# Performance work log

Hardware: AMD Instinct MI355X
Metric: run time of the kernel (lower is better)

## Reference

```python
import jax, jax.numpy as jnp
import numpy as np
from jax import lax

B, L, T, CH, H = 32, 40960, 12, 512, 256  # batch, audio len, timestep, enc ch, gru hidden


def _conv_bn_relu(x, w, stride, pad, g, be):
    y = lax.conv_general_dilated(x, w, (stride,), [(pad, pad)],
                                 dimension_numbers=('NCH', 'OIH', 'NCH'))
    m = jnp.mean(y, axis=(0, 2), keepdims=True)          # train-mode BatchNorm1d
    v = jnp.var(y, axis=(0, 2), keepdims=True)
    y = (y - m) / jnp.sqrt(v + 1e-5) * g[None, :, None] + be[None, :, None]
    return jax.nn.relu(y)


def _gru(xs, wih, whh, bih, bhh):
    # xs: [B, F, I] -> outputs [B, F, H]; PyTorch GRU equations
    def step(h, x_t):
        gi = x_t @ wih.T + bih
        gh = h @ whh.T + bhh
        ir, iz, inn = jnp.split(gi, 3, axis=-1)
        hr, hz, hn = jnp.split(gh, 3, axis=-1)
        r = jax.nn.sigmoid(ir + hr)
        zg = jax.nn.sigmoid(iz + hz)
        n = jnp.tanh(inn + r * hn)
        h_new = (1 - zg) * n + zg * h
        return h_new, h_new
    h0 = jnp.zeros((xs.shape[0], whh.shape[1]), xs.dtype)
    _, ys = lax.scan(step, h0, jnp.swapaxes(xs, 0, 1))
    return jnp.swapaxes(ys, 0, 1)


def setup_inputs():
    ks = jax.random.split(jax.random.key(0), 16)
    x = jax.random.normal(ks[0], (B, 1, L), jnp.float32)
    seq_lens = jax.random.randint(ks[1], (B,), L // 2, L + 1)
    maxt = seq_lens // 160 - T                            # t ~ randint(seq_len/160 - timestep)
    u = jax.random.uniform(ks[2], (B,))
    t_samples = jnp.minimum((u * maxt).astype(jnp.int32), maxt - 1)
    d = {'x': x, 't_samples': t_samples}
    d['w1'] = jax.random.normal(ks[3], (CH, 1, 10), jnp.float32) * 0.1
    d['w2'] = jax.random.normal(ks[4], (CH, CH, 8), jnp.float32) * 0.03
    d['w3'] = jax.random.normal(ks[5], (CH, CH, 4), jnp.float32) * 0.05
    d['w4'] = jax.random.normal(ks[6], (CH, CH, 4), jnp.float32) * 0.05
    d['w5'] = jax.random.normal(ks[7], (CH, CH, 4), jnp.float32) * 0.05
    for i in range(5):
        d[f'g{i+1}'] = jnp.ones((CH,), jnp.float32)
        d[f'be{i+1}'] = jnp.zeros((CH,), jnp.float32)
    d['wih'] = jax.random.normal(ks[8], (3 * H, CH), jnp.float32) * 0.05
    d['whh'] = jax.random.normal(ks[9], (3 * H, H), jnp.float32) * 0.05
    d['bih'] = jnp.zeros((3 * H,), jnp.float32)
    d['bhh'] = jnp.zeros((3 * H,), jnp.float32)
    d['wk'] = jax.random.normal(ks[10], (T, CH, H), jnp.float32) * 0.05
    d['bk'] = jnp.zeros((T, CH), jnp.float32)
    return d


def reference(x, t_samples, w1, w2, w3, w4, w5, g1, g2, g3, g4, g5,
              be1, be2, be3, be4, be5, wih, whh, bih, bhh, wk, bk):
    z = _conv_bn_relu(x, w1, 5, 3, g1, be1)
    z = _conv_bn_relu(z, w2, 4, 2, g2, be2)
    z = _conv_bn_relu(z, w3, 2, 1, g3, be3)
    z = _conv_bn_relu(z, w4, 2, 1, g4, be4)
    z = _conv_bn_relu(z, w5, 2, 1, g5, be5)
    z = jnp.swapaxes(z, 1, 2)                              # [B, F, CH]
    # encode_samples: z at t+1 .. t+T  -> [T, B, CH]
    idx = t_samples[:, None] + jnp.arange(1, T + 1)[None, :]   # [B, T]
    enc = jnp.take_along_axis(z, idx[:, :, None], axis=1)      # [B, T, CH]
    enc = jnp.swapaxes(enc, 0, 1)                              # [T, B, CH]
    # zero-padded forward sequence (GRU is causal, so output at t only sees prefix)
    mask = (jnp.arange(z.shape[1])[None, :] <= t_samples[:, None]).astype(z.dtype)
    out = _gru(z * mask[:, :, None], wih, whh, bih, bhh)       # [B, F, H]
    c_t = out[jnp.arange(out.shape[0]), t_samples]             # [B, H]
    pred = jnp.einsum('bh,tdh->tbd', c_t, wk) + bk[:, None, :]  # [T, B, CH]
    totals = jnp.einsum('tbd,tcd->tbc', enc, pred)             # [T, B, B]
    lsm = jax.nn.log_softmax(totals, axis=2)                   # torch LogSoftmax dim=1 on 2D
    nce = jnp.trace(lsm, axis1=1, axis2=2).sum() / (-1.0 * B * T)
    preds = jnp.argmax(jax.nn.softmax(totals, axis=2), axis=1)  # argmax over dim 0 per column
    correct = jnp.sum(preds == jnp.arange(B)[None, :])
    accuracy = correct / B
    return (accuracy, nce)
```

## Files before the change

### kernel.cpp

```cpp
#include <hip/hip_runtime.h>
#include <hip/hip_bf16.h>


using bf16 = __hip_bfloat16;
typedef __attribute__((ext_vector_type(8))) short bf16x8;
typedef __attribute__((ext_vector_type(4))) float f32x4;

__device__ __forceinline__ float bf2f(bf16 v) { return __bfloat162float(v); }
__device__ __forceinline__ bf16 f2bf(float f) { return __float2bfloat16(f); }
__device__ __forceinline__ ushort bfbits(float f) {
  bf16 b = f2bf(f);
  return *reinterpret_cast<ushort*>(&b);
}
union FragU { uint4 u; bf16x8 v; };

__global__ __launch_bounds__(256) void stats1_kernel(
    const float* __restrict__ x, const float* __restrict__ w1, float* __restrict__ sums) {
  __shared__ float xs[2576];
  int s = blockIdx.x, b = blockIdx.y;
  const float* xb = x + (size_t)b * 40960;
  int w0 = 2560 * s - 3;
  for (int i = threadIdx.x; i < 2565; i += 256) {
    int xi = w0 + i;
    xs[i] = ((unsigned)xi < 40960u) ? xb[xi] : 0.f;
  }
  __syncthreads();
  int c0 = threadIdx.x, c1 = threadIdx.x + 256;
  float wA[10], wB[10];
#pragma unroll
  for (int k = 0; k < 10; ++k) { wA[k] = w1[c0 * 10 + k]; wB[k] = w1[c1 * 10 + k]; }
  float sA = 0.f, qA = 0.f, sB = 0.f, qB = 0.f;
  for (int f = 0; f < 512; ++f) {
    const float* xp = &xs[5 * f];
    float aA = 0.f, aB = 0.f;
#pragma unroll
    for (int k = 0; k < 10; ++k) {
      float xv = xp[k];
      aA = fmaf(xv, wA[k], aA);
      aB = fmaf(xv, wB[k], aB);
    }
    sA += aA; qA = fmaf(aA, aA, qA);
    sB += aB; qB = fmaf(aB, aB, qB);
  }
  atomicAdd(&sums[c0], sA); atomicAdd(&sums[512 + c0], qA);
  atomicAdd(&sums[c1], sB); atomicAdd(&sums[512 + c1], qB);
}

__global__ __launch_bounds__(256) void stats_kernel(
    const bf16* __restrict__ z, int F, float* __restrict__ sums) {
  int bc = blockIdx.x;
  int c = bc & 511;
  const bf16* p = z + (size_t)bc * F;
  float s = 0.f, q = 0.f;
  for (int i = threadIdx.x; i < F; i += 256) {
    float v = bf2f(p[i]);
    s += v;
    q = fmaf(v, v, q);
  }
  __shared__ float rs[256], rq[256];
  rs[threadIdx.x] = s; rq[threadIdx.x] = q;
  __syncthreads();
  for (int w = 128; w > 0; w >>= 1) {
    if (threadIdx.x < w) {
      rs[threadIdx.x] += rs[threadIdx.x + w];
      rq[threadIdx.x] += rq[threadIdx.x + w];
    }
    __syncthreads();
  }
  if (threadIdx.x == 0) {
    atomicAdd(&sums[c], rs[0]);
    atomicAdd(&sums[512 + c], rq[0]);
  }
}

__global__ void finalize_kernel(const float* __restrict__ sums, const float* __restrict__ g,
                                const float* __restrict__ be, float invN,
                                float* __restrict__ ab) {
  int c = threadIdx.x;
  float mean = sums[c] * invN;
  float var = fmaf(-mean, mean, sums[512 + c] * invN);
  float a = g[c] * rsqrtf(var + 1e-5f);
  ab[c] = a;
  ab[512 + c] = fmaf(-mean, a, be[c]);
}

__global__ __launch_bounds__(256) void transpose_kernel(
    const float* __restrict__ in, float* __restrict__ out, int R, int C) {
  __shared__ float t[64][65];
  int c0 = blockIdx.x * 64, r0 = blockIdx.y * 64;
  int tx = threadIdx.x & 63, ty = threadIdx.x >> 6;
  for (int i = ty; i < 64; i += 4) {
    int r = r0 + i, c = c0 + tx;
    t[i][tx] = (r < R && c < C) ? in[(size_t)r * C + c] : 0.f;
  }
  __syncthreads();
  for (int i = ty; i < 64; i += 4) {
    int c = c0 + i, r = r0 + tx;
    if (c < C && r < R) out[(size_t)c * R + r] = t[tx][i];
  }
}

__global__ void cvt_bf16_kernel(const float* __restrict__ in, bf16* __restrict__ out, int n) {
  int i = blockIdx.x * 256 + threadIdx.x;
  if (i < n) out[i] = f2bf(in[i]);
}

__global__ void pack_whh_kernel(const float* __restrict__ whh, uint* __restrict__ P) {
  int idx = blockIdx.x * 256 + threadIdx.x;
  if (idx < 98304) {
    int p = idx / 768, gj = idx % 768;
    float lo = whh[(size_t)gj * 256 + 2 * p];
    float hi = whh[(size_t)gj * 256 + 2 * p + 1];
    P[idx] = (uint)bfbits(lo) | ((uint)bfbits(hi) << 16);
  }
}

__global__ __launch_bounds__(256) void norm1_kernel(
    const float* __restrict__ x, const float* __restrict__ w1,
    const float* __restrict__ ab, bf16* __restrict__ zn, int chunk0) {
  __shared__ float xs[1312];
  int s = blockIdx.x, bl = blockIdx.y;
  int pidx = s * 256 + threadIdx.x;
  const float* xb = x + (size_t)(chunk0 + bl) * 40960;
  int w0 = 1280 * s - 33;
  for (int i = threadIdx.x; i < 1285; i += 256) {
    int xi = w0 + i;
    xs[i] = ((unsigned)xi < 40960u) ? xb[xi] : 0.f;
  }
  __syncthreads();
  if (pidx >= 8208) return;
  int fi = pidx - 6;
  bool inb = ((unsigned)fi < 8192u);
  const float* xp = &xs[5 * threadIdx.x];
  bf16* zp = zn + (size_t)bl * 512 * 8208 + pidx;
  for (int c = 0; c < 512; ++c) {
    float v = 0.f;
    if (inb) {
      float acc = 0.f;
      const float* w = &w1[c * 10];
#pragma unroll
      for (int k = 0; k < 10; ++k) acc = fmaf(xp[k], w[k], acc);
      v = fmaxf(fmaf(ab[c], acc, ab[512 + c]), 0.f);
    }
    zp[(size_t)c * 8208] = f2bf(v);
  }
}

__global__ __launch_bounds__(256) void conv2_mfma(
    const bf16* __restrict__ zn, const bf16* __restrict__ wB,
    bf16* __restrict__ out, int chunk0) {
  __shared__ ushort aL[4][520];
  __shared__ ushort bL[128][36];
  int fo0 = blockIdx.x * 128, co0 = blockIdx.y * 128, bl = blockIdx.z;
  int tid = threadIdx.x;
  int w = tid >> 6, l = tid & 63;
  int m0 = (w >> 1) * 64, n0 = (w & 1) * 64;
  int row = l & 15, kq = l >> 4;
  f32x4 acc[4][4];
#pragma unroll
  for (int i = 0; i < 4; ++i)
#pragma unroll
    for (int j = 0; j < 4; ++j) acc[i][j] = {0.f, 0.f, 0.f, 0.f};
  const ushort* zb = (const ushort*)zn + (size_t)bl * 512 * 8208;
  int astart = 4 * fo0 + 4;
  int sco = tid >> 1, shalf = tid & 1;
  for (int step = 0; step < 128; ++step) {
    int ci0 = step * 4;
    int k0 = step * 32;
    __syncthreads();
    for (int u = tid; u < 520; u += 256) {
      int ci = u / 130, off = (u % 130) * 4;
      *(uint2*)&aL[ci][off] =
          *(const uint2*)(zb + (size_t)(ci0 + ci) * 8208 + astart + off);
    }
    {
      const uint2* src = (const uint2*)(wB + (size_t)(co0 + sco) * 4096 + k0 + shalf * 16);
      uint2* dst = (uint2*)&bL[sco][shalf * 16];
      dst[0] = src[0]; dst[1] = src[1]; dst[2] = src[2]; dst[3] = src[3];
    }
    __syncthreads();
    bf16x8 af[4], bfr[4];
#pragma unroll
    for (int mi = 0; mi < 4; ++mi) {
      int am = (m0 + mi * 16 + row) * 4;
      const uint2* ap = (const uint2*)((const char*)&aL[0][0] + kq * 1040 + am * 2);
      uint2 a0 = ap[0], a1 = ap[1];
      FragU f; f.u = make_uint4(a0.x, a0.y, a1.x, a1.y);
      af[mi] = f.v;
    }
#pragma unroll
    for (int ni = 0; ni < 4; ++ni) {
      int col = n0 + ni * 16 + row;
      const uint2* bp = (const uint2*)((const char*)&bL[0][0] + col * 72 + kq * 16);
      uint2 b0 = bp[0], b1 = bp[1];
      FragU f; f.u = make_uint4(b0.x, b0.y, b1.x, b1.y);
      bfr[ni] = f.v;
    }
#pragma unroll
    for (int mi = 0; mi < 4; ++mi)
#pragma unroll
      for (int ni = 0; ni < 4; ++ni)
        acc[mi][ni] = __builtin_amdgcn_mfma_f32_16x16x32_bf16(af[mi], bfr[ni], acc[mi][ni], 0, 0, 0);
  }
  size_t ob = (size_t)(chunk0 + bl) * 512;
#pragma unroll
  for (int mi = 0; mi < 4; ++mi)
#pragma unroll
    for (int ni = 0; ni < 4; ++ni)
#pragma unroll
      for (int r = 0; r < 4; ++r) {
        int m = m0 + mi * 16 + kq * 4 + r;
        int n = n0 + ni * 16 + row;
        out[(ob + co0 + n) * 2048 + fo0 + m] = f2bf(acc[mi][ni][r]);
      }
}

__global__ __launch_bounds__(256) void convN_mfma(
    const bf16* __restrict__ in, const bf16* __restrict__ wB,
    const float* __restrict__ ab, bf16* __restrict__ out, int Fi, int Fo) {
  __shared__ ushort aL[8][264];
  __shared__ ushort bL[128][36];
  int fo0 = blockIdx.x * 128, co0 = blockIdx.y * 128, b = blockIdx.z;
  int tid = threadIdx.x;
  int w = tid >> 6, l = tid & 63;
  int m0 = (w >> 1) * 64, n0 = (w & 1) * 64;
  int row = l & 15, kq = l >> 4;
  f32x4 acc[4][4];
#pragma unroll
  for (int i = 0; i < 4; ++i)
#pragma unroll
    for (int j = 0; j < 4; ++j) acc[i][j] = {0.f, 0.f, 0.f, 0.f};
  int fi0 = fo0 * 2 - 1;
  const bf16* ib = in + (size_t)b * 512 * Fi;
  int sco = tid >> 1, shalf = tid & 1;
  for (int step = 0; step < 64; ++step) {
    int ci0 = step * 8;
    int k0 = step * 32;
    __syncthreads();
    for (int u = tid; u < 1032; u += 256) {
      int ci = u / 129, pp = (u % 129) * 2;
      float a = ab[ci0 + ci], bb = ab[512 + ci0 + ci];
      const bf16* zr = ib + (size_t)(ci0 + ci) * Fi;
      uint pk = 0;
#pragma unroll
      for (int e = 0; e < 2; ++e) {
        int fi = fi0 + pp + e;
        float v = 0.f;
        if ((unsigned)fi < (unsigned)Fi)
          v = fmaxf(fmaf(a, bf2f(zr[fi]), bb), 0.f);
        pk |= (uint)bfbits(v) << (16 * e);
      }
      *(uint*)&aL[ci][pp] = pk;
    }
    {
      const uint2* src = (const uint2*)(wB + (size_t)(co0 + sco) * 2048 + k0 + shalf * 16);
      uint2* dst = (uint2*)&bL[sco][shalf * 16];
      dst[0] = src[0]; dst[1] = src[1]; dst[2] = src[2]; dst[3] = src[3];
    }
    __syncthreads();
    bf16x8 af[4], bfr[4];
#pragma unroll
    for (int mi = 0; mi < 4; ++mi) {
      int p0 = (m0 + mi * 16 + row) * 2;
      const char* base = (const char*)&aL[0][0];
      const uint* r0p = (const uint*)(base + (2 * kq) * 528 + p0 * 2);
      const uint* r1p = (const uint*)(base + (2 * kq + 1) * 528 + p0 * 2);
      FragU f; f.u = make_uint4(r0p[0], r0p[1], r1p[0], r1p[1]);
      af[mi] = f.v;
    }
#pragma unroll
    for (int ni = 0; ni < 4; ++ni) {
      int col = n0 + ni * 16 + row;
      const uint2* bp = (const uint2*)((const char*)&bL[0][0] + col * 72 + kq * 16);
      uint2 b0 = bp[0], b1 = bp[1];
      FragU f; f.u = make_uint4(b0.x, b0.y, b1.x, b1.y);
      bfr[ni] = f.v;
    }
#pragma unroll
    for (int mi = 0; mi < 4; ++mi)
#pragma unroll
      for (int ni = 0; ni < 4; ++ni)
        acc[mi][ni] = __builtin_amdgcn_mfma_f32_16x16x32_bf16(af[mi], bfr[ni], acc[mi][ni], 0, 0, 0);
  }
  size_t ob = (size_t)b * 512;
#pragma unroll
  for (int mi = 0; mi < 4; ++mi)
#pragma unroll
    for (int ni = 0; ni < 4; ++ni)
#pragma unroll
      for (int r = 0; r < 4; ++r) {
        int m = m0 + mi * 16 + kq * 4 + r;
        int n = n0 + ni * 16 + row;
        out[(ob + co0 + n) * Fo + fo0 + m] = f2bf(acc[mi][ni][r]);
      }
}

__global__ __launch_bounds__(256) void gi_kernel(
    const bf16* __restrict__ z5, const float* __restrict__ wihT,
    const float* __restrict__ bih, const float* __restrict__ ab,
    float* __restrict__ gi) {
  __shared__ float a_lds[8][64];
  __shared__ float w_lds[8][128];
  int t0 = blockIdx.x * 64, j0 = blockIdx.y * 128, b = blockIdx.z;
  int tid = threadIdx.x, tx = tid & 15, ty = tid >> 4;
  float acc[4][8] = {};
  for (int ci0 = 0; ci0 < 512; ci0 += 8) {
    __syncthreads();
    for (int i = tid; i < 512; i += 256) {
      int ci = i >> 6, t = i & 63;
      float v = bf2f(z5[((size_t)b * 512 + ci0 + ci) * 256 + t0 + t]);
      a_lds[ci][t] = fmaxf(fmaf(ab[ci0 + ci], v, ab[512 + ci0 + ci]), 0.f);
    }
    {
      int i = tid * 4;
      int ci = i >> 7, j = i & 127;
      *(float4*)&w_lds[ci][j] = *(const float4*)&wihT[(size_t)(ci0 + ci) * 768 + j0 + j];
    }
    __syncthreads();
#pragma unroll
    for (int ci = 0; ci < 8; ++ci) {
      float av[4];
#pragma unroll
      for (int j = 0; j < 4; ++j) av[j] = a_lds[ci][tx + 16 * j];
      const float* wp = &w_lds[ci][ty * 8];
      float4 w0 = *(const float4*)wp;
      float4 w1 = *(const float4*)(wp + 4);
      float wv[8] = {w0.x, w0.y, w0.z, w0.w, w1.x, w1.y, w1.z, w1.w};
#pragma unroll
      for (int j = 0; j < 4; ++j)
#pragma unroll
        for (int cc = 0; cc < 8; ++cc)
          acc[j][cc] = fmaf(av[j], wv[cc], acc[j][cc]);
    }
  }
  float bv[8];
#pragma unroll
  for (int cc = 0; cc < 8; ++cc) bv[cc] = bih[j0 + ty * 8 + cc];
#pragma unroll
  for (int j = 0; j < 4; ++j) {
    int rowi = t0 + tx + 16 * j;
    float4 s0 = {acc[j][0] + bv[0], acc[j][1] + bv[1], acc[j][2] + bv[2], acc[j][3] + bv[3]};
    float4 s1 = {acc[j][4] + bv[4], acc[j][5] + bv[5], acc[j][6] + bv[6], acc[j][7] + bv[7]};
    float* gp = &gi[((size_t)b * 256 + rowi) * 768 + j0 + ty * 8];
    *(float4*)gp = s0;
    *(float4*)(gp + 4) = s1;
  }
}

__global__ __launch_bounds__(256) void gru_kernel(
    const float* __restrict__ gi, const uint* __restrict__ P,
    const float* __restrict__ bhh, const int* __restrict__ tsamp,
    float* __restrict__ c_t) {
  int b = blockIdx.x;
  int j = threadIdx.x;
  __shared__ float h[256];
  h[j] = 0.f;
  int Tb = tsamp[b];
  float bhr = bhh[j], bhz = bhh[256 + j], bhn = bhh[512 + j];
  const float* gib = gi + (size_t)b * 256 * 768;
  __syncthreads();
  for (int t = 0; t <= Tb; ++t) {
    const float* git = gib + t * 768;
    float dr = 0.f, dz = 0.f, dn = 0.f;
#pragma unroll 4
    for (int p = 0; p < 128; ++p) {
      uint ur = P[p * 768 + j];
      uint uz = P[p * 768 + 256 + j];
      uint un = P[p * 768 + 512 + j];
      float2 hh = *(const float2*)&h[2 * p];
      dr = fmaf(__uint_as_float(ur << 16), hh.x, dr);
      dr = fmaf(__uint_as_float(ur & 0xffff0000u), hh.y, dr);
      dz = fmaf(__uint_as_float(uz << 16), hh.x, dz);
      dz = fmaf(__uint_as_float(uz & 0xffff0000u), hh.y, dz);
      dn = fmaf(__uint_as_float(un << 16), hh.x, dn);
      dn = fmaf(__uint_as_float(un & 0xffff0000u), hh.y, dn);
    }
    float xr_ = git[j], xz_ = git[256 + j], xn_ = git[512 + j];
    float r = 1.f / (1.f + __expf(-(xr_ + dr + bhr)));
    float zg = 1.f / (1.f + __expf(-(xz_ + dz + bhz)));
    float n = tanhf(fmaf(r, dn + bhn, xn_));
    float hj = h[j];
    float hnew = fmaf(zg, hj - n, n);
    __syncthreads();
    h[j] = hnew;
    __syncthreads();
  }
  c_t[b * 256 + j] = h[j];
}

__global__ __launch_bounds__(256) void pred_kernel(
    const float* __restrict__ c_t, const float* __restrict__ wk,
    const float* __restrict__ bk, float* __restrict__ pred) {
  int tp = blockIdx.x >> 5, c = blockIdx.x & 31;
  __shared__ float cl[256];
  cl[threadIdx.x] = c_t[c * 256 + threadIdx.x];
  __syncthreads();
  const float* wkt = wk + (size_t)tp * 512 * 256;
  for (int d = threadIdx.x; d < 512; d += 256) {
    float a = bk[tp * 512 + d];
    const float* wv = wkt + (size_t)d * 256;
    for (int hh = 0; hh < 256; hh += 4) {
      float4 w4 = *(const float4*)&wv[hh];
      a = fmaf(w4.x, cl[hh], a);
      a = fmaf(w4.y, cl[hh + 1], a);
      a = fmaf(w4.z, cl[hh + 2], a);
      a = fmaf(w4.w, cl[hh + 3], a);
    }
    pred[((size_t)tp * 32 + c) * 512 + d] = a;
  }
}

__global__ __launch_bounds__(256) void totals_kernel(
    const bf16* __restrict__ z5, const float* __restrict__ ab,
    const int* __restrict__ tsamp, const float* __restrict__ pred,
    float* __restrict__ totals) {
  int tp = blockIdx.x >> 5, b = blockIdx.x & 31;
  __shared__ float el[512];
  __shared__ float red[256];
  int tb = tsamp[b] + 1 + tp;
  for (int d = threadIdx.x; d < 512; d += 256) {
    float v = bf2f(z5[((size_t)b * 512 + d) * 256 + tb]);
    el[d] = fmaxf(fmaf(ab[d], v, ab[512 + d]), 0.f);
  }
  __syncthreads();
  int c = threadIdx.x & 31, chunk = threadIdx.x >> 5;
  const float* pr = pred + ((size_t)tp * 32 + c) * 512 + chunk * 64;
  const float* ep = &el[chunk * 64];
  float a = 0.f;
#pragma unroll 8
  for (int d = 0; d < 64; ++d) a = fmaf(pr[d], ep[d], a);
  red[threadIdx.x] = a;
  __syncthreads();
  if (threadIdx.x < 32) {
    float s = 0.f;
#pragma unroll
    for (int k = 0; k < 8; ++k) s += red[k * 32 + threadIdx.x];
    totals[((size_t)tp * 32 + b) * 32 + threadIdx.x] = s;
  }
}

__global__ __launch_bounds__(384) void final_kernel(const float* __restrict__ totals,
                                                    float* __restrict__ out) {
  __shared__ float adj[12 * 32 * 32];
  __shared__ float tr_red[384];
  __shared__ int cr_red[384];
  int tid = threadIdx.x;
  for (int i = tid; i < 12288; i += 384) adj[i] = totals[i];
  __syncthreads();
  int tp = tid / 32, b = tid % 32;
  float* row = &adj[(tp * 32 + b) * 32];
  float mx = row[0];
#pragma unroll
  for (int c = 1; c < 32; ++c) mx = fmaxf(mx, row[c]);
  float se = 0.f;
  for (int c = 0; c < 32; ++c) se += expf(row[c] - mx);
  float lse = mx + logf(se);
  float tr = row[b] - lse;
  __syncthreads();
  for (int c = 0; c < 32; ++c) row[c] -= lse;
  __syncthreads();
  int c = b;
  float best = adj[(tp * 32 + 0) * 32 + c];
  int bi = 0;
  for (int bb = 1; bb < 32; ++bb) {
    float v = adj[(tp * 32 + bb) * 32 + c];
    if (v > best) { best = v; bi = bb; }
  }
  tr_red[tid] = tr;
  cr_red[tid] = (bi == c) ? 1 : 0;
  __syncthreads();
  if (tid == 0) {
    float ts_ = 0.f;
    int cs = 0;
    for (int i = 0; i < 384; ++i) { ts_ += tr_red[i]; cs += cr_red[i]; }
    out[0] = (float)cs / 32.0f;
    out[1] = ts_ / (-384.0f);
  }
}

extern "C" void kernel_launch(void* const* d_in, const int* in_sizes, int n_in,
                              void* d_out, int out_size, void* d_ws, size_t ws_size,
                              hipStream_t stream) {
  const float* x = (const float*)d_in[0];
  const int* tsamp = (const int*)d_in[1];
  const float* w1 = (const float*)d_in[2];
  const float* w2 = (const float*)d_in[3];
  const float* w3 = (const float*)d_in[4];
  const float* w4 = (const float*)d_in[5];
  const float* w5 = (const float*)d_in[6];
  const float* gg[5] = {(const float*)d_in[7], (const float*)d_in[9], (const float*)d_in[11],
                        (const float*)d_in[13], (const float*)d_in[15]};
  const float* bee[5] = {(const float*)d_in[8], (const float*)d_in[10], (const float*)d_in[12],
                         (const float*)d_in[14], (const float*)d_in[16]};
  const float* wih = (const float*)d_in[17];
  const float* whh = (const float*)d_in[18];
  const float* bih = (const float*)d_in[19];
  const float* bhh = (const float*)d_in[20];
  const float* wk = (const float*)d_in[21];
  const float* bk = (const float*)d_in[22];
  float* out = (float*)d_out;

  char* base = (char*)d_ws;
  size_t off = 0;
  auto alloc = [&](size_t bytes) -> char* {
    char* r = base + off;
    off = (off + bytes + 255) & ~(size_t)255;
    return r;
  };
  char* S1 = alloc((size_t)8 * 512 * 8208 * 2);
  char* S2 = alloc((size_t)32 * 512 * 2048 * 2);
  bf16* z1n = (bf16*)S1;
  bf16* z2r = (bf16*)S2;
  bf16* z3r = (bf16*)S1;
  bf16* z4r = (bf16*)S2;
  float* gi = (float*)S1;
  bf16* z5 = (bf16*)alloc((size_t)4194304 * 2);
  bf16* wB2 = (bf16*)alloc((size_t)2097152 * 2);
  bf16* wB3 = (bf16*)alloc((size_t)1048576 * 2);
  bf16* wB4 = (bf16*)alloc((size_t)1048576 * 2);
  bf16* wB5 = (bf16*)alloc((size_t)1048576 * 2);
  float* wihT = (float*)alloc((size_t)393216 * 4);
  uint* whhP = (uint*)alloc((size_t)98304 * 4);
  float* stats = (float*)alloc(5 * 1024 * 4);
  float* ab = (float*)alloc(5 * 1024 * 4);
  float* ct = (float*)alloc(8192 * 4);
  float* pred = (float*)alloc(196608 * 4);
  float* totals = (float*)alloc(12288 * 4);
  (void)ws_size;

  hipMemsetAsync(stats, 0, 5 * 1024 * 4, stream);

  cvt_bf16_kernel<<<8192, 256, 0, stream>>>(w2, wB2, 2097152);
  cvt_bf16_kernel<<<4096, 256, 0, stream>>>(w3, wB3, 1048576);
  cvt_bf16_kernel<<<4096, 256, 0, stream>>>(w4, wB4, 1048576);
  cvt_bf16_kernel<<<4096, 256, 0, stream>>>(w5, wB5, 1048576);
  transpose_kernel<<<dim3(8, 12), 256, 0, stream>>>(wih, wihT, 768, 512);
  pack_whh_kernel<<<384, 256, 0, stream>>>(whh, whhP);

  stats1_kernel<<<dim3(16, 32), 256, 0, stream>>>(x, w1, stats);
  finalize_kernel<<<1, 512, 0, stream>>>(stats, gg[0], bee[0], 1.f / 262144.f, ab);

  for (int ch = 0; ch < 4; ++ch) {
    norm1_kernel<<<dim3(33, 8), 256, 0, stream>>>(x, w1, ab, z1n, ch * 8);
    conv2_mfma<<<dim3(16, 4, 8), 256, 0, stream>>>(z1n, wB2, z2r, ch * 8);
  }
  stats_kernel<<<16384, 256, 0, stream>>>(z2r, 2048, stats + 1024);
  finalize_kernel<<<1, 512, 0, stream>>>(stats + 1024, gg[1], bee[1], 1.f / 65536.f, ab + 1024);

  convN_mfma<<<dim3(8, 4, 32), 256, 0, stream>>>(z2r, wB3, ab + 1024, z3r, 2048, 1024);
  stats_kernel<<<16384, 256, 0, stream>>>(z3r, 1024, stats + 2048);
  finalize_kernel<<<1, 512, 0, stream>>>(stats + 2048, gg[2], bee[2], 1.f / 32768.f, ab + 2048);

  convN_mfma<<<dim3(4, 4, 32), 256, 0, stream>>>(z3r, wB4, ab + 2048, z4r, 1024, 512);
  stats_kernel<<<16384, 256, 0, stream>>>(z4r, 512, stats + 3072);
  finalize_kernel<<<1, 512, 0, stream>>>(stats + 3072, gg[3], bee[3], 1.f / 16384.f, ab + 3072);

  convN_mfma<<<dim3(2, 4, 32), 256, 0, stream>>>(z4r, wB5, ab + 3072, z5, 512, 256);
  stats_kernel<<<16384, 256, 0, stream>>>(z5, 256, stats + 4096);
  finalize_kernel<<<1, 512, 0, stream>>>(stats + 4096, gg[4], bee[4], 1.f / 8192.f, ab + 4096);

  gi_kernel<<<dim3(4, 6, 32), 256, 0, stream>>>(z5, wihT, bih, ab + 4096, gi);
  gru_kernel<<<32, 256, 0, stream>>>(gi, whhP, bhh, tsamp, ct);
  pred_kernel<<<384, 256, 0, stream>>>(ct, wk, bk, pred);
  totals_kernel<<<384, 256, 0, stream>>>(z5, ab + 4096, tsamp, pred, totals);
  final_kernel<<<1, 384, 0, stream>>>(totals, out);
}
```

Baseline: 3.950 ms.

## Keep GRU recurrent weights in registers and split the hidden dot product across two thread halves

The GRU kernel now runs 512 threads per batch row. Each half of the block keeps its share of the packed bf16 W_hh columns (192 uints per thread) in registers instead of reloading them from global memory every timestep. The two partial dot products are combined through shared memory before the gate math. The weight packing is reordered to match. This removes repeated global or L2 weight traffic in the serial recurrence, but the large register arrays risk spills and lower occupancy.

```diff
diff --git a/kernel.cpp b/kernel.cpp
--- a/kernel.cpp
+++ b/kernel.cpp
@@ -105,13 +105,15 @@
   if (i < n) out[i] = f2bf(in[i]);
 }
 
-__global__ void pack_whh_kernel(const float* __restrict__ whh, uint* __restrict__ P) {
+__global__ void pack_whh_kernel(const float* __restrict__ whh, uint* __restrict__ P2) {
   int idx = blockIdx.x * 256 + threadIdx.x;
   if (idx < 98304) {
-    int p = idx / 768, gj = idx % 768;
-    float lo = whh[(size_t)gj * 256 + 2 * p];
-    float hi = whh[(size_t)gj * 256 + 2 * p + 1];
-    P[idx] = (uint)bfbits(lo) | ((uint)bfbits(hi) << 16);
+    int qcc = idx / 768, gj = idx % 768;
+    int q = qcc >> 6, cc = qcc & 63;
+    int c0 = 128 * q + 2 * cc;
+    float lo = whh[(size_t)gj * 256 + c0];
+    float hi = whh[(size_t)gj * 256 + c0 + 1];
+    P2[idx] = (uint)bfbits(lo) | ((uint)bfbits(hi) << 16);
   }
 }
 
@@ -347,45 +349,65 @@
   }
 }
 
-__global__ __launch_bounds__(256) void gru_kernel(
-    const float* __restrict__ gi, const uint* __restrict__ P,
+__global__ __launch_bounds__(512) void gru_kernel(
+    const float* __restrict__ gi, const uint* __restrict__ P2,
     const float* __restrict__ bhh, const int* __restrict__ tsamp,
     float* __restrict__ c_t) {
   int b = blockIdx.x;
-  int j = threadIdx.x;
-  __shared__ float h[256];
-  h[j] = 0.f;
+  int tid = threadIdx.x;
+  int q = tid >> 8, j = tid & 255;
+  __shared__ float hs[256];
+  __shared__ float pr[512], pz[512], pn[512];
+  uint W[192];
+  {
+    const uint* Pq = P2 + (size_t)q * 64 * 768 + j;
+#pragma unroll
+    for (int g = 0; g < 3; ++g)
+#pragma unroll
+      for (int cc = 0; cc < 64; ++cc)
+        W[g * 64 + cc] = Pq[cc * 768 + g * 256];
+  }
+  if (tid < 256) hs[tid] = 0.f;
   int Tb = tsamp[b];
   float bhr = bhh[j], bhz = bhh[256 + j], bhn = bhh[512 + j];
   const float* gib = gi + (size_t)b * 256 * 768;
   __syncthreads();
   for (int t = 0; t <= Tb; ++t) {
-    const float* git = gib + t * 768;
-    float dr = 0.f, dz = 0.f, dn = 0.f;
-#pragma unroll 4
-    for (int p = 0; p < 128; ++p) {
-      uint ur = P[p * 768 + j];
-      uint uz = P[p * 768 + 256 + j];
-      uint un = P[p * 768 + 512 + j];
-      float2 hh = *(const float2*)&h[2 * p];
-      dr = fmaf(__uint_as_float(ur << 16), hh.x, dr);
-      dr = fmaf(__uint_as_float(ur & 0xffff0000u), hh.y, dr);
-      dz = fmaf(__uint_as_float(uz << 16), hh.x, dz);
-      dz = fmaf(__uint_as_float(uz & 0xffff0000u), hh.y, dz);
-      dn = fmaf(__uint_as_float(un << 16), hh.x, dn);
-      dn = fmaf(__uint_as_float(un & 0xffff0000u), hh.y, dn);
-    }
-    float xr_ = git[j], xz_ = git[256 + j], xn_ = git[512 + j];
-    float r = 1.f / (1.f + __expf(-(xr_ + dr + bhr)));
-    float zg = 1.f / (1.f + __expf(-(xz_ + dz + bhz)));
-    float n = tanhf(fmaf(r, dn + bhn, xn_));
-    float hj = h[j];
-    float hnew = fmaf(zg, hj - n, n);
-    __syncthreads();
-    h[j] = hnew;
-    __syncthreads();
-  }
-  c_t[b * 256 + j] = h[j];
+    float xr_ = 0.f, xz_ = 0.f, xn_ = 0.f;
+    if (tid < 256) {
+      const float* git = gib + t * 768;
+      xr_ = git[j]; xz_ = git[256 + j]; xn_ = git[512 + j];
+    }
+    float2 ar = {0.f, 0.f}, az = {0.f, 0.f}, an = {0.f, 0.f};
+    const float2* h2 = (const float2*)hs + q * 64;
+#pragma unroll
+    for (int cc = 0; cc < 64; ++cc) {
+      float2 hh = h2[cc];
+      uint ur = W[cc], uz = W[64 + cc], un = W[128 + cc];
+      ar.x = fmaf(__uint_as_float(ur << 16), hh.x, ar.x);
+      ar.y = fmaf(__uint_as_float(ur & 0xffff0000u), hh.y, ar.y);
+      az.x = fmaf(__uint_as_float(uz << 16), hh.x, az.x);
+      az.y = fmaf(__uint_as_float(uz & 0xffff0000u), hh.y, az.y);
+      an.x = fmaf(__uint_as_float(un << 16), hh.x, an.x);
+      an.y = fmaf(__uint_as_float(un & 0xffff0000u), hh.y, an.y);
+    }
+    pr[tid] = ar.x + ar.y;
+    pz[tid] = az.x + az.y;
+    pn[tid] = an.x + an.y;
+    __syncthreads();
+    if (tid < 256) {
+      float sr = pr[j] + pr[j + 256];
+      float sz = pz[j] + pz[j + 256];
+      float sn = pn[j] + pn[j + 256];
+      float r = 1.f / (1.f + __expf(-(xr_ + sr + bhr)));
+      float zg = 1.f / (1.f + __expf(-(xz_ + sz + bhz)));
+      float n = tanhf(fmaf(r, sn + bhn, xn_));
+      float hj = hs[j];
+      hs[j] = fmaf(zg, hj - n, n);
+    }
+    __syncthreads();
+  }
+  if (tid < 256) c_t[b * 256 + j] = hs[j];
 }
 
 __global__ __launch_bounds__(256) void pred_kernel(
@@ -560,7 +582,7 @@
   finalize_kernel<<<1, 512, 0, stream>>>(stats + 4096, gg[4], bee[4], 1.f / 8192.f, ab + 4096);
 
   gi_kernel<<<dim3(4, 6, 32), 256, 0, stream>>>(z5, wihT, bih, ab + 4096, gi);
-  gru_kernel<<<32, 256, 0, stream>>>(gi, whhP, bhh, tsamp, ct);
+  gru_kernel<<<32, 512, 0, stream>>>(gi, whhP, bhh, tsamp, ct);
   pred_kernel<<<384, 256, 0, stream>>>(ct, wk, bk, pred);
   totals_kernel<<<384, 256, 0, stream>>>(z5, ab + 4096, tsamp, pred, totals);
   final_kernel<<<1, 384, 0, stream>>>(totals, out);
```

Measured after the change: 4.676 ms. +18.4%, slower.
